# Optimization experiments

Measured on AMD Instinct MI355X. Metric: run time of the kernel, lower is better.

The kernel has to match this reference:

```python
import jax, jax.numpy as jnp
import numpy as np
from jax.scipy.special import gammaln, logsumexp

T, BATCH = 500, 64
S, A, OBS, CTL, H = 64, 16, 32, 8, 30


def _scale_tril(lv, tl):
    # lv [K,D], tl [K,D,D] -> lower-triangular L with exp(lv) on the diagonal
    D = lv.shape[-1]
    return jnp.tril(tl, -1) + jnp.exp(lv)[..., None] * jnp.eye(D, dtype=lv.dtype)


def mvn_logprob(x, mu, lv, tl):
    # x [T,B,D], mixture of K full-cov MVNs (mu [K,D]) -> logp [T,B,K]
    D = mu.shape[-1]
    L = _scale_tril(lv, tl)  # [K,D,D]
    eye = jnp.eye(D, dtype=x.dtype)
    Linv = jax.vmap(lambda l: jax.scipy.linalg.solve_triangular(l, eye, lower=True))(L)
    diff = x[:, :, None, :] - mu  # [T,B,K,D] (dominant intermediate)
    z = jnp.einsum('kij,tbkj->tbki', Linv, diff)
    return -0.5 * jnp.sum(z * z, -1) - jnp.sum(lv, -1) - 0.5 * D * jnp.log(2.0 * jnp.pi)


def reference(o, u, obs_mu, obs_lv, obs_tl, ctl_mu, ctl_lv, ctl_tl, B_logits, D_logits, C_logits, tau):
    logp_o = mvn_logprob(o, obs_mu, obs_lv, obs_tl)  # [T,B,S]
    logp_u = mvn_logprob(u, ctl_mu, ctl_lv, ctl_tl)  # [T,B,A]
    p_a = jax.nn.softmax(logp_u, -1)
    Bp = jax.nn.softmax(B_logits, -1)  # [A,S,S] transition probs
    b0 = jnp.broadcast_to(jax.nn.softmax(D_logits, -1), logp_o.shape[1:])  # [B,S]

    def hmm_step(b, inp):
        lo, pa = inp  # [B,S], [B,A]
        prior = jnp.einsum('na,asj,ns->nj', pa, Bp, b)  # action-averaged predict
        lik = jnp.exp(lo - jnp.max(lo, -1, keepdims=True))  # stable, normalization cancels
        post = lik * prior
        bn = post / jnp.sum(post, -1, keepdims=True)
        return bn, bn

    _, b_seq = jax.lax.scan(hmm_step, b0, (logp_o, p_a))
    b = jnp.concatenate([b0[None], b_seq])  # [T+1,B,S]

    # reward R = -KL(B || C) - obs entropy (literal torch: sum(B*logB - logC, -1))
    obs_ent = 0.5 * OBS * (1.0 + jnp.log(2.0 * jnp.pi)) + jnp.sum(obs_lv, -1)  # [S]
    Cp = jax.nn.softmax(C_logits, -1)  # [S]
    kl = jnp.sum(Bp * jnp.log(Bp) - jnp.log(Cp), -1)  # [A,S]
    R = -kl - obs_ent[None, :]  # [A,S]

    def vi_step(Q, _):
        V = logsumexp(Q, axis=0)  # soft-max over actions -> [S]
        Qn = R + jnp.einsum('asj,j->as', Bp, V)
        return Qn, Qn

    _, Qs = jax.lax.scan(vi_step, R, None, length=H - 1)
    Qh = jnp.concatenate([R[None], Qs])  # [H,A,S]

    rate = jnp.exp(tau[0, 0])
    k = jnp.arange(H, dtype=o.dtype)
    logh = k * jnp.log(rate) - rate - gammaln(k + 1.0)
    h = jax.nn.softmax(logh)  # normalized (truncated) Poisson horizon pdf
    Q = jnp.einsum('h,has->as', h, Qh)  # [A,S]

    G = jnp.einsum('tns,as->tna', b[:-1], Q)  # expected free energy per action
    logp_pi = logsumexp(jax.nn.log_softmax(G, -1) + logp_u, -1)  # [T,B]
    logp_b = jnp.log(b[1:] + 1e-6)
    logp_obs = logsumexp(logp_b * logp_o, -1)  # [T,B] (literal to torch source)
    return logp_pi, logp_obs


def setup_inputs() -> dict:
    key = jax.random.key(0)
    ks = jax.random.split(key, 12)
    f = jnp.float32
    return {
        'o': jax.random.normal(ks[0], (T, BATCH, OBS), f),
        'u': jax.random.normal(ks[1], (T, BATCH, CTL), f),
        'obs_mu': jax.random.normal(ks[2], (S, OBS), f),
        'obs_lv': 0.1 * jax.random.normal(ks[3], (S, OBS), f),
        'obs_tl': 0.1 * jax.random.normal(ks[4], (S, OBS, OBS), f),
        'ctl_mu': jax.random.normal(ks[5], (A, CTL), f),
        'ctl_lv': 0.1 * jax.random.normal(ks[6], (A, CTL), f),
        'ctl_tl': 0.1 * jax.random.normal(ks[7], (A, CTL, CTL), f),
        'B_logits': jax.random.normal(ks[8], (A, S, S), f),
        'D_logits': jax.random.normal(ks[9], (S,), f),
        'C_logits': jax.random.normal(ks[10], (S,), f),
        'tau': 0.5 * jax.random.normal(ks[11], (1, 1), f),
    }
```

## Files before the change

### kernel.cpp

```cpp
#include <hip/hip_runtime.h>
#include <math.h>

#define T_STEPS 500
#define BATCH   64
#define S_DIM   64
#define A_DIM   16
#define OBS_D   32
#define CTL_D   8
#define H_DIM   30

#define CHUNKS   8
#define CHUNK_L  63
#define BURN     16
#define MAXSTEPS (CHUNK_L + BURN)

#define LOG2PI 1.8378770664093453f

typedef _Float16 v2h __attribute__((ext_vector_type(2)));
typedef __fp16  fp16x2 __attribute__((ext_vector_type(2)));

__device__ __forceinline__ float wmax(float v){
  #pragma unroll
  for (int o = 32; o > 0; o >>= 1) v = fmaxf(v, __shfl_xor(v, o, 64));
  return v;
}
__device__ __forceinline__ float wsum(float v){
  #pragma unroll
  for (int o = 32; o > 0; o >>= 1) v += __shfl_xor(v, o, 64);
  return v;
}

template<int CTRL>
__device__ __forceinline__ float dpp_add(float v){
  int x = __builtin_amdgcn_update_dpp(0, __float_as_int(v), CTRL, 0xF, 0xF, true);
  return v + __int_as_float(x);
}
__device__ __forceinline__ v2h u2h(unsigned int x){
  union { unsigned int u; v2h h; } c; c.u = x; return c.h;
}
__device__ __forceinline__ unsigned int pack_pkrtz(float a, float b){
  union { fp16x2 h; unsigned int u; } c;
  c.h = __builtin_amdgcn_cvt_pkrtz(a, b);
  return c.u;
}

#define BAR() do { \
  asm volatile("s_waitcnt lgkmcnt(0)" ::: "memory"); \
  __builtin_amdgcn_s_barrier(); \
  asm volatile("" ::: "memory"); \
  __builtin_amdgcn_sched_barrier(0); \
} while (0)

#define FOR16(X) X(0) X(1) X(2) X(3) X(4) X(5) X(6) X(7) X(8) X(9) X(10) X(11) X(12) X(13) X(14) X(15)

__global__ __launch_bounds__(256) void k_front(const float* __restrict__ o,
                                               const float* __restrict__ obs_mu,
                                               const float* __restrict__ obs_lv,
                                               const float* __restrict__ obs_tl,
                                               const float* __restrict__ Blog,
                                               const float* __restrict__ u,
                                               const float* __restrict__ ctl_mu,
                                               const float* __restrict__ ctl_lv,
                                               const float* __restrict__ ctl_tl,
                                               float* __restrict__ lo_out,
                                               _Float16* __restrict__ Bph,
                                               float* __restrict__ lup,
                                               float* __restrict__ pap){
  const int bx  = blockIdx.x;
  const int tid = threadIdx.x;

  if (bx < 8000){
    const int k = bx & 63;
    const float* __restrict__ Lk  = obs_tl + k * OBS_D * OBS_D;
    const float* __restrict__ muk = obs_mu + k * OBS_D;
    const float* __restrict__ lvk = obs_lv + k * OBS_D;

    float dinv[OBS_D];
    float lvsum = 0.f;
    #pragma unroll
    for (int i = 0; i < OBS_D; ++i){
      float x = lvk[i];
      lvsum += x;
      dinv[i] = __expf(-x);
    }

    const int item = (bx >> 6) * 256 + tid;
    const float* op = o + item * OBS_D;
    float d[OBS_D];
    #pragma unroll
    for (int i = 0; i < OBS_D; i += 4){
      float4 v = *(const float4*)(op + i);
      d[i]   = v.x - muk[i];
      d[i+1] = v.y - muk[i+1];
      d[i+2] = v.z - muk[i+2];
      d[i+3] = v.w - muk[i+3];
    }
    float z[OBS_D];
    float acc = 0.f;
    #pragma unroll
    for (int i = 0; i < OBS_D; ++i){
      float s0 = d[i], s1 = 0.f;
      #pragma unroll
      for (int jj = 0; jj + 1 < i; jj += 2){
        s0 = fmaf(-Lk[i * OBS_D + jj],     z[jj],     s0);
        s1 = fmaf(-Lk[i * OBS_D + jj + 1], z[jj + 1], s1);
      }
      if (i & 1) s0 = fmaf(-Lk[i * OBS_D + i - 1], z[i - 1], s0);
      float zz = (s0 + s1) * dinv[i];
      z[i] = zz;
      acc  = fmaf(zz, zz, acc);
    }
    lo_out[item * S_DIM + k] = -0.5f * acc - lvsum - 0.5f * OBS_D * LOG2PI;
    return;
  }

  if (bx < 8256){
    const int row  = (bx - 8000) * 4 + (tid >> 6);
    const int lane = tid & 63;
    float v = Blog[row * 64 + lane];
    float m = wmax(v);
    float e = __expf(v - m);
    float s = wsum(e);
    const int a  = row >> 6;
    const int ss = row & 63;
    Bph[(a * 64 + lane) * 64 + ss] = (_Float16)(e / s);
    return;
  }

  const int item = (bx - 8256) * 256 + tid;
  const float* up = u + item * CTL_D;
  float uu[CTL_D];
  #pragma unroll
  for (int i = 0; i < CTL_D; i += 4){
    float4 v = *(const float4*)(up + i);
    uu[i] = v.x; uu[i+1] = v.y; uu[i+2] = v.z; uu[i+3] = v.w;
  }
  float lp[A_DIM];
  #pragma unroll
  for (int a = 0; a < A_DIM; ++a){
    float z[CTL_D];
    float acc = 0.f, lvs = 0.f;
    #pragma unroll
    for (int i = 0; i < CTL_D; ++i){
      float lvv = ctl_lv[a * CTL_D + i];
      lvs += lvv;
      float s = uu[i] - ctl_mu[a * CTL_D + i];
      #pragma unroll
      for (int jj = 0; jj < i; ++jj) s = fmaf(-ctl_tl[a * 64 + i * CTL_D + jj], z[jj], s);
      z[i] = s * __expf(-lvv);
      acc  = fmaf(z[i], z[i], acc);
    }
    lp[a] = -0.5f * acc - lvs - 0.5f * CTL_D * LOG2PI;
  }
  float m = -1e30f;
  #pragma unroll
  for (int a = 0; a < A_DIM; ++a) m = fmaxf(m, lp[a]);
  float e[A_DIM], se = 0.f;
  #pragma unroll
  for (int a = 0; a < A_DIM; ++a){ e[a] = __expf(lp[a] - m); se += e[a]; }
  float inv = 1.f / se;
  #pragma unroll
  for (int a = 0; a < A_DIM; ++a){
    lup[item * A_DIM + a] = lp[a];
    pap[item * A_DIM + a] = e[a] * inv;
  }
}

__global__ __launch_bounds__(1024, 1) void k_vi(const float* __restrict__ Blog,
                                                const float* __restrict__ obs_lv,
                                                const float* __restrict__ Clog,
                                                const float* __restrict__ tau,
                                                float* __restrict__ Qout){
  const int tid  = threadIdx.x;
  const int lane = tid & 63;
  __shared__ __align__(16) float Vs[S_DIM];
  __shared__ __align__(16) float Qlds[A_DIM][S_DIM];
  __shared__ float hs[H_DIM];

  float c  = Clog[lane];
  float cm = wmax(c);
  float cs = wsum(__expf(c - cm));
  float lseC = cm + __logf(cs);
  float sumLnCp = wsum(c) - 64.f * lseC;

  if (tid < 64){
    float t0   = tau[0];
    float rate = __expf(t0);
    float lg = 0.f;
    for (int i = 2; i <= lane; ++i) lg += __logf((float)i);
    float lh = (lane < H_DIM) ? ((float)lane * t0 - rate - lg) : -1e30f;
    float m  = wmax(lh);
    float e  = (lane < H_DIM) ? __expf(lh - m) : 0.f;
    float s  = wsum(e);
    if (lane < H_DIM) hs[lane] = e / s;
  }

  const int r = tid;
  const int a = r >> 6, s = r & 63;
  const float* p = Blog + r * 64;
  float4 raw[16];
  float mr = -1e30f;
  #pragma unroll
  for (int q = 0; q < 16; ++q){
    float4 v = *(const float4*)(p + 4 * q);
    raw[q] = v;
    mr = fmaxf(mr, fmaxf(fmaxf(v.x, v.y), fmaxf(v.z, v.w)));
  }
  float ssum = 0.f, dot = 0.f;
  #pragma unroll
  for (int q = 0; q < 16; ++q){
    float4 v = raw[q];
    float4 e;
    e.x = __expf(v.x - mr); e.y = __expf(v.y - mr);
    e.z = __expf(v.z - mr); e.w = __expf(v.w - mr);
    ssum += (e.x + e.y) + (e.z + e.w);
    dot  += e.x * (v.x - mr) + e.y * (v.y - mr) + e.z * (v.z - mr) + e.w * (v.w - mr);
    raw[q] = e;
  }
  float inv = 1.f / ssum;
  float lns = __logf(ssum);
  #pragma unroll
  for (int q = 0; q < 16; ++q){
    float4 e = raw[q];
    raw[q] = make_float4(e.x * inv, e.y * inv, e.z * inv, e.w * inv);
  }
  float negent = dot * inv - lns;

  float oe = 0.f;
  const float* lvp = obs_lv + s * OBS_D;
  #pragma unroll
  for (int dd = 0; dd < OBS_D; dd += 4){
    float4 v = *(const float4*)(lvp + dd);
    oe += v.x + v.y + v.z + v.w;
  }
  oe += 0.5f * OBS_D * (1.f + LOG2PI);
  float R  = -negent + sumLnCp - oe;
  float Qc = R;
  __syncthreads();
  float Qa = hs[0] * R;

  for (int it = 1; it < H_DIM; ++it){
    Qlds[a][s] = Qc;
    __syncthreads();
    if (tid < 64){
      float m = -1e30f;
      #pragma unroll
      for (int aa = 0; aa < A_DIM; ++aa) m = fmaxf(m, Qlds[aa][lane]);
      float sv = 0.f;
      #pragma unroll
      for (int aa = 0; aa < A_DIM; ++aa) sv += __expf(Qlds[aa][lane] - m);
      Vs[lane] = m + __logf(sv);
    }
    __syncthreads();
    float hw = hs[it];
    float accA = 0.f, accB = 0.f;
    #pragma unroll
    for (int q = 0; q < 16; ++q){
      float4 v = *(const float4*)(&Vs[4 * q]);
      accA = fmaf(raw[q].x, v.x, fmaf(raw[q].y, v.y, accA));
      accB = fmaf(raw[q].z, v.z, fmaf(raw[q].w, v.w, accB));
    }
    Qc = R + accA + accB;
    Qa = fmaf(hw, Qc, Qa);
  }
  Qout[r] = Qa;
}

__global__ __launch_bounds__(512, 4)
void k_scan(const _Float16* __restrict__ Bph,
            const float* __restrict__ lo,
            const float* __restrict__ pa,
            const float* __restrict__ Dlog,
            float* __restrict__ bseq){
  const int n   = blockIdx.x;
  const int c   = blockIdx.y;
  const int tid = threadIdx.x;
  const int g   = tid >> 6;
  const int l   = tid & 63;
  const int so  = l & 7;
  const int jj  = l >> 3;
  const int j   = g * 8 + jj;

  const int t_out0  = c * CHUNK_L;
  const int t_end   = (t_out0 + CHUNK_L < T_STEPS) ? (t_out0 + CHUNK_L) : T_STEPS;
  const int t_start = (c == 0) ? 0 : (t_out0 - BURN);
  const int nsteps  = t_end - t_start;

  __shared__ __align__(16) float lik_lds[MAXSTEPS][S_DIM];
  __shared__ __align__(16) unsigned int b16[2][32];
  __shared__ __align__(16) unsigned short ps16[2][8];

  #define DECLT(A) uint4 Tq##A;
  FOR16(DECLT)
  #define LOADT(A) Tq##A = *(const uint4*)(Bph + ((A) * 4096 + j * 64 + 8 * so));
  FOR16(LOADT)
  #define PINT(A) asm volatile("" : "+v"(Tq##A.x), "+v"(Tq##A.y), "+v"(Tq##A.z), "+v"(Tq##A.w));
  FOR16(PINT)

  const float* lo_n = lo + n * 64;
  const float* pa_n = pa + n * 16;
  for (int i = tid; i < nsteps * 64; i += 512){
    int r = i >> 6, col = i & 63;
    lik_lds[r][col] = lo_n[(t_start + r) * 4096 + col];
  }
  if (tid < 64){
    float dl = (c == 0) ? Dlog[l] : 0.f;
    float m = wmax(dl);
    float e = __expf(dl - m);
    float s = wsum(e);
    float b0 = e / s;
    if (c == 0) bseq[n * 64 + l] = b0;
    float nb = __shfl_xor(b0, 1, 64);
    if (!(l & 1)) b16[0][l >> 1] = pack_pkrtz(b0, nb);
  }
  if (tid < 8) ps16[0][tid] = 0x3000;
  __syncthreads();

  for (int r = g; r < nsteps; r += 8){
    float v = lik_lds[r][l];
    float m = wmax(v);
    lik_lds[r][l] = __expf(v - m);
  }
  __syncthreads();

  #define DECLPA(A) float pac_##A, pan_##A;
  FOR16(DECLPA)
  const float* pp0 = pa_n + t_start * 1024;
  #define LDPA0(A) pac_##A = pp0[A];
  FOR16(LDPA0)

  int cur = 0;
  for (int tt = 0; tt < nsteps; ++tt){
    const int t   = t_start + tt;
    const int nxt = cur ^ 1;

    const int t1 = (t + 1 < T_STEPS) ? (t + 1) : (T_STEPS - 1);
    const float* pp1 = pa_n + t1 * 1024;
    #define LDPAN(A) pan_##A = pp1[A];
    FOR16(LDPAN)

    float likr = lik_lds[tt][j];
    uint4 q = *(const uint4*)&ps16[cur][0];
    v2h a01 = u2h(q.x) + u2h(q.y);
    v2h a23 = u2h(q.z) + u2h(q.w);
    v2h aa  = a01 + a23;
    float sum = (float)aa.x + (float)aa.y;
    float lik = likr * __builtin_amdgcn_rcpf(sum);

    uint4 bq = *(const uint4*)&b16[cur][so * 4];
    v2h bh0 = u2h(bq.x), bh1 = u2h(bq.y), bh2 = u2h(bq.z), bh3 = u2h(bq.w);

    float pr0 = 0.f, pr1 = 0.f, pr2 = 0.f, pr3 = 0.f;
    #define DOTQ(A, P) { \
      float y = __builtin_amdgcn_fdot2(u2h(Tq##A.x), bh0, \
                __builtin_amdgcn_fdot2(u2h(Tq##A.y), bh1, \
                __builtin_amdgcn_fdot2(u2h(Tq##A.z), bh2, \
                __builtin_amdgcn_fdot2(u2h(Tq##A.w), bh3, 0.f, false), false), false), false); \
      P = fmaf(pac_##A, y, P); }
    DOTQ(0,  pr0) DOTQ(1,  pr1) DOTQ(2,  pr2) DOTQ(3,  pr3)
    DOTQ(4,  pr0) DOTQ(5,  pr1) DOTQ(6,  pr2) DOTQ(7,  pr3)
    DOTQ(8,  pr0) DOTQ(9,  pr1) DOTQ(10, pr2) DOTQ(11, pr3)
    DOTQ(12, pr0) DOTQ(13, pr1) DOTQ(14, pr2) DOTQ(15, pr3)
    float pri = (pr0 + pr1) + (pr2 + pr3);

    pri = dpp_add<0xB1>(pri);
    pri = dpp_add<0x4E>(pri);
    pri = dpp_add<0x141>(pri);

    float post = pri * lik;
    if (t >= t_out0){
      if (so == 0)
        bseq[(t + 1) * 4096 + n * 64 + j] = post;
    }

    {
      int x = __builtin_amdgcn_update_dpp(0, __float_as_int(post), 0x128, 0xF, 0xF, true);
      if (!(l & 15)) b16[nxt][g * 4 + (l >> 4)] = pack_pkrtz(post, __int_as_float(x));
    }

    {
      float w = post;
      w = dpp_add<0x128>(w);
      w = dpp_add<0x142>(w);
      w = dpp_add<0x143>(w);
      if (l == 48) ps16[nxt][g] = (unsigned short)(pack_pkrtz(w, 0.f) & 0xffffu);
    }

    #define CPPA(A) pac_##A = pan_##A;
    FOR16(CPPA)

    BAR();
    cur = nxt;
  }
}

__global__ __launch_bounds__(256, 1) void k_out(const float* __restrict__ bseq,
                                                const float* __restrict__ Qg,
                                                const float* __restrict__ lo,
                                                const float* __restrict__ lu,
                                                float* __restrict__ out){
  __shared__ __align__(16) float Qs[A_DIM][S_DIM];
  const int tid = threadIdx.x;
  for (int i = tid; i < A_DIM * S_DIM; i += 256) Qs[i >> 6][i & 63] = Qg[i];
  __syncthreads();

  const int item = blockIdx.x * 256 + tid;
  float bs[64];
  const float* bp_ = bseq + item * 64;
  float bsum = 0.f;
  #pragma unroll
  for (int i = 0; i < 16; ++i){
    float4 v = *(const float4*)(bp_ + 4 * i);
    bs[4*i] = v.x; bs[4*i+1] = v.y; bs[4*i+2] = v.z; bs[4*i+3] = v.w;
    bsum += (v.x + v.y) + (v.z + v.w);
  }
  float binv = 1.0f / bsum;

  float G[A_DIM];
  #pragma unroll
  for (int a = 0; a < A_DIM; ++a){
    float acc = 0.f;
    #pragma unroll
    for (int s = 0; s < 64; ++s) acc = fmaf(bs[s], Qs[a][s], acc);
    G[a] = acc * binv;
  }
  const float* lup = lu + item * A_DIM;
  float m1 = -1e30f, m0 = -1e30f;
  float x1[A_DIM];
  #pragma unroll
  for (int a = 0; a < A_DIM; ++a){
    x1[a] = G[a] + lup[a];
    m1 = fmaxf(m1, x1[a]);
    m0 = fmaxf(m0, G[a]);
  }
  float e1 = 0.f, e0 = 0.f;
  #pragma unroll
  for (int a = 0; a < A_DIM; ++a){
    e1 += __expf(x1[a] - m1);
    e0 += __expf(G[a] - m0);
  }
  out[item] = (m1 + __logf(e1)) - (m0 + __logf(e0));

  const float* bq = bseq + (item + 64) * 64;
  float bsum2 = 0.f;
  #pragma unroll
  for (int i = 0; i < 16; ++i){
    float4 v = *(const float4*)(bq + 4 * i);
    bs[4*i] = v.x; bs[4*i+1] = v.y; bs[4*i+2] = v.z; bs[4*i+3] = v.w;
    bsum2 += (v.x + v.y) + (v.z + v.w);
  }
  float inv2 = 1.0f / bsum2;
  const float* lop = lo + item * 64;
  float terms[64];
  float mt = -1e30f;
  #pragma unroll
  for (int i = 0; i < 16; ++i){
    float4 v = *(const float4*)(lop + 4 * i);
    float t0 = __logf(bs[4*i]   * inv2 + 1e-6f) * v.x;
    float t1 = __logf(bs[4*i+1] * inv2 + 1e-6f) * v.y;
    float t2 = __logf(bs[4*i+2] * inv2 + 1e-6f) * v.z;
    float t3 = __logf(bs[4*i+3] * inv2 + 1e-6f) * v.w;
    terms[4*i] = t0; terms[4*i+1] = t1; terms[4*i+2] = t2; terms[4*i+3] = t3;
    mt = fmaxf(mt, fmaxf(fmaxf(t0, t1), fmaxf(t2, t3)));
  }
  float es = 0.f;
  #pragma unroll
  for (int s = 0; s < 64; ++s) es += __expf(terms[s] - mt);
  out[T_STEPS * BATCH + item] = mt + __logf(es);
}

extern "C" void kernel_launch(void* const* d_in, const int* in_sizes, int n_in,
                              void* d_out, int out_size, void* d_ws, size_t ws_size,
                              hipStream_t stream){
  const float* o      = (const float*)d_in[0];
  const float* u      = (const float*)d_in[1];
  const float* obs_mu = (const float*)d_in[2];
  const float* obs_lv = (const float*)d_in[3];
  const float* obs_tl = (const float*)d_in[4];
  const float* ctl_mu = (const float*)d_in[5];
  const float* ctl_lv = (const float*)d_in[6];
  const float* ctl_tl = (const float*)d_in[7];
  const float* Blog   = (const float*)d_in[8];
  const float* Dlog   = (const float*)d_in[9];
  const float* Clog   = (const float*)d_in[10];
  const float* tau    = (const float*)d_in[11];
  float* out = (float*)d_out;
  float* ws  = (float*)d_ws;

  _Float16* Bph = (_Float16*)ws;
  float* Q    = ws + 32768;
  float* lo   = ws + 33792;
  float* lu   = ws + 2081792;
  float* pa   = ws + 2593792;
  float* bseq = ws + 3105792;

  k_front<<<8381, 256, 0, stream>>>(o, obs_mu, obs_lv, obs_tl, Blog,
                                    u, ctl_mu, ctl_lv, ctl_tl, lo, Bph, lu, pa);
  k_vi   <<<1, 1024, 0, stream>>>(Blog, obs_lv, Clog, tau, Q);
  k_scan <<<dim3(64, CHUNKS), 512, 0, stream>>>(Bph, lo, pa, Dlog, bseq);
  k_out  <<<125, 256, 0, stream>>>(bseq, Q, lo, lu, out);
}
```

Measured before the change: 200.6 us.

## Fuse output reduction into scan kernel using LDS belief history

The output kernel is folded into the chunked scan kernel. Each block keeps its chunk's beliefs and raw observation log-likelihoods in shared memory, then computes the policy and observation log-probabilities with wave shuffles. This removes the global bseq round-trip and one kernel launch. In exchange it adds roughly 37KB of LDS per block, which with the launch bound relaxed may lower occupancy, and it adds a serial epilogue after the scan in each block.

```diff
diff --git a/kernel.cpp b/kernel.cpp
--- a/kernel.cpp
+++ b/kernel.cpp
@@ -266,12 +266,14 @@
   Qout[r] = Qa;
 }
 
-__global__ __launch_bounds__(512, 4)
+__global__ __launch_bounds__(512)
 void k_scan(const _Float16* __restrict__ Bph,
             const float* __restrict__ lo,
             const float* __restrict__ pa,
             const float* __restrict__ Dlog,
-            float* __restrict__ bseq){
+            const float* __restrict__ lu,
+            const float* __restrict__ Qg,
+            float* __restrict__ out){
   const int n   = blockIdx.x;
   const int c   = blockIdx.y;
   const int tid = threadIdx.x;
@@ -285,8 +287,12 @@
   const int t_end   = (t_out0 + CHUNK_L < T_STEPS) ? (t_out0 + CHUNK_L) : T_STEPS;
   const int t_start = (c == 0) ? 0 : (t_out0 - BURN);
   const int nsteps  = t_end - t_start;
+  const int burnoff = t_out0 - t_start;
 
   __shared__ __align__(16) float lik_lds[MAXSTEPS][S_DIM];
+  __shared__ __align__(16) float lo_raw[CHUNK_L][S_DIM];
+  __shared__ __align__(16) float hist[CHUNK_L + 1][S_DIM];
+  __shared__ __align__(16) float Qs[A_DIM][S_DIM];
   __shared__ __align__(16) unsigned int b16[2][32];
   __shared__ __align__(16) unsigned short ps16[2][8];
 
@@ -303,13 +309,15 @@
     int r = i >> 6, col = i & 63;
     lik_lds[r][col] = lo_n[(t_start + r) * 4096 + col];
   }
+  for (int i = tid; i < A_DIM * S_DIM; i += 512)
+    Qs[i >> 6][i & 63] = Qg[i];
   if (tid < 64){
     float dl = (c == 0) ? Dlog[l] : 0.f;
     float m = wmax(dl);
     float e = __expf(dl - m);
     float s = wsum(e);
     float b0 = e / s;
-    if (c == 0) bseq[n * 64 + l] = b0;
+    if (c == 0) hist[0][l] = b0;
     float nb = __shfl_xor(b0, 1, 64);
     if (!(l & 1)) b16[0][l >> 1] = pack_pkrtz(b0, nb);
   }
@@ -318,6 +326,7 @@
 
   for (int r = g; r < nsteps; r += 8){
     float v = lik_lds[r][l];
+    if (r >= burnoff) lo_raw[r - burnoff][l] = v;
     float m = wmax(v);
     lik_lds[r][l] = __expf(v - m);
   }
@@ -368,9 +377,8 @@
     pri = dpp_add<0x141>(pri);
 
     float post = pri * lik;
-    if (t >= t_out0){
-      if (so == 0)
-        bseq[(t + 1) * 4096 + n * 64 + j] = post;
+    if (t >= t_out0 - 1){
+      if (so == 0) hist[t - t_out0 + 1][j] = post;
     }
 
     {
@@ -392,81 +400,46 @@
     BAR();
     cur = nxt;
   }
-}
-
-__global__ __launch_bounds__(256, 1) void k_out(const float* __restrict__ bseq,
-                                                const float* __restrict__ Qg,
-                                                const float* __restrict__ lo,
-                                                const float* __restrict__ lu,
-                                                float* __restrict__ out){
-  __shared__ __align__(16) float Qs[A_DIM][S_DIM];
-  const int tid = threadIdx.x;
-  for (int i = tid; i < A_DIM * S_DIM; i += 256) Qs[i >> 6][i & 63] = Qg[i];
   __syncthreads();
 
-  const int item = blockIdx.x * 256 + tid;
-  float bs[64];
-  const float* bp_ = bseq + item * 64;
-  float bsum = 0.f;
-  #pragma unroll
-  for (int i = 0; i < 16; ++i){
-    float4 v = *(const float4*)(bp_ + 4 * i);
-    bs[4*i] = v.x; bs[4*i+1] = v.y; bs[4*i+2] = v.z; bs[4*i+3] = v.w;
-    bsum += (v.x + v.y) + (v.z + v.w);
-  }
-  float binv = 1.0f / bsum;
-
-  float G[A_DIM];
-  #pragma unroll
-  for (int a = 0; a < A_DIM; ++a){
-    float acc = 0.f;
-    #pragma unroll
-    for (int s = 0; s < 64; ++s) acc = fmaf(bs[s], Qs[a][s], acc);
-    G[a] = acc * binv;
-  }
-  const float* lup = lu + item * A_DIM;
-  float m1 = -1e30f, m0 = -1e30f;
-  float x1[A_DIM];
-  #pragma unroll
-  for (int a = 0; a < A_DIM; ++a){
-    x1[a] = G[a] + lup[a];
-    m1 = fmaxf(m1, x1[a]);
-    m0 = fmaxf(m0, G[a]);
-  }
-  float e1 = 0.f, e0 = 0.f;
-  #pragma unroll
-  for (int a = 0; a < A_DIM; ++a){
-    e1 += __expf(x1[a] - m1);
-    e0 += __expf(G[a] - m0);
-  }
-  out[item] = (m1 + __logf(e1)) - (m0 + __logf(e0));
-
-  const float* bq = bseq + (item + 64) * 64;
-  float bsum2 = 0.f;
-  #pragma unroll
-  for (int i = 0; i < 16; ++i){
-    float4 v = *(const float4*)(bq + 4 * i);
-    bs[4*i] = v.x; bs[4*i+1] = v.y; bs[4*i+2] = v.z; bs[4*i+3] = v.w;
-    bsum2 += (v.x + v.y) + (v.z + v.w);
-  }
-  float inv2 = 1.0f / bsum2;
-  const float* lop = lo + item * 64;
-  float terms[64];
-  float mt = -1e30f;
-  #pragma unroll
-  for (int i = 0; i < 16; ++i){
-    float4 v = *(const float4*)(lop + 4 * i);
-    float t0 = __logf(bs[4*i]   * inv2 + 1e-6f) * v.x;
-    float t1 = __logf(bs[4*i+1] * inv2 + 1e-6f) * v.y;
-    float t2 = __logf(bs[4*i+2] * inv2 + 1e-6f) * v.z;
-    float t3 = __logf(bs[4*i+3] * inv2 + 1e-6f) * v.w;
-    terms[4*i] = t0; terms[4*i+1] = t1; terms[4*i+2] = t2; terms[4*i+3] = t3;
-    mt = fmaxf(mt, fmaxf(fmaxf(t0, t1), fmaxf(t2, t3)));
-  }
-  float es = 0.f;
-  #pragma unroll
-  for (int s = 0; s < 64; ++s) es += __expf(terms[s] - mt);
-  out[T_STEPS * BATCH + item] = mt + __logf(es);
+  const int a_ = l & 15;
+  const int sg = l >> 4;
+  for (int t = t_out0 + g; t < t_end; t += 8){
+    const int ht = t - t_out0;
+    float acc = 0.f, bsumA = 0.f;
+    #pragma unroll
+    for (int i = 0; i < 16; ++i){
+      float bv = hist[ht][sg * 16 + i];
+      acc    = fmaf(bv, Qs[a_][sg * 16 + i], acc);
+      bsumA += bv;
+    }
+    acc   += __shfl_xor(acc, 16, 64);   acc   += __shfl_xor(acc, 32, 64);
+    bsumA += __shfl_xor(bsumA, 16, 64); bsumA += __shfl_xor(bsumA, 32, 64);
+    float G  = acc / bsumA;
+    float luv = lu[(t * 64 + n) * 16 + a_];
+    float x1 = G + luv;
+    float m1 = x1, m0 = G;
+    #pragma unroll
+    for (int o = 1; o < 16; o <<= 1){
+      m1 = fmaxf(m1, __shfl_xor(m1, o, 64));
+      m0 = fmaxf(m0, __shfl_xor(m0, o, 64));
+    }
+    float e1 = __expf(x1 - m1), e0 = __expf(G - m0);
+    #pragma unroll
+    for (int o = 1; o < 16; o <<= 1){
+      e1 += __shfl_xor(e1, o, 64);
+      e0 += __shfl_xor(e0, o, 64);
+    }
+    if (l == 0) out[t * 64 + n] = (m1 + __logf(e1)) - (m0 + __logf(e0));
+
+    float b1 = hist[ht + 1][l];
+    float bsumB = wsum(b1);
+    float bn = b1 / bsumB;
+    float term = __logf(bn + 1e-6f) * lo_raw[ht][l];
+    float mt = wmax(term);
+    float es = wsum(__expf(term - mt));
+    if (l == 0) out[T_STEPS * BATCH + t * 64 + n] = mt + __logf(es);
+  }
 }
 
 extern "C" void kernel_launch(void* const* d_in, const int* in_sizes, int n_in,
@@ -492,11 +465,9 @@
   float* lo   = ws + 33792;
   float* lu   = ws + 2081792;
   float* pa   = ws + 2593792;
-  float* bseq = ws + 3105792;
 
   k_front<<<8381, 256, 0, stream>>>(o, obs_mu, obs_lv, obs_tl, Blog,
                                     u, ctl_mu, ctl_lv, ctl_tl, lo, Bph, lu, pa);
   k_vi   <<<1, 1024, 0, stream>>>(Blog, obs_lv, Clog, tau, Q);
-  k_scan <<<dim3(64, CHUNKS), 512, 0, stream>>>(Bph, lo, pa, Dlog, bseq);
-  k_out  <<<125, 256, 0, stream>>>(bseq, Q, lo, lu, out);
-}
+  k_scan <<<dim3(64, CHUNKS), 512, 0, stream>>>(Bph, lo, pa, Dlog, lu, Q, out);
+}
```

Measured after the change: 201.6 us. No clear change (+0.5%).
